# Kernel optimization log

Measured on AMD Instinct MI355X. Metric: run time of the kernel, lower is better.

Reference implementation:

```python
import jax, jax.numpy as jnp
import numpy as np

RATIO = 0.5  # init arg of CAGPool_layer
B, N_PER_GRAPH, D, DEG = 256, 512, 256, 32


def setup_inputs() -> dict:
    key = jax.random.key(0)
    k1, k2, k3, k4 = jax.random.split(key, 4)
    N = B * N_PER_GRAPH
    Eg = N_PER_GRAPH * DEG  # edges per graph
    x = jax.random.normal(k1, (N, D), dtype=jnp.float32)
    # within-graph random edges, then offset to global node ids
    src = jax.random.randint(k2, (B, Eg), 0, N_PER_GRAPH, dtype=jnp.int32)
    dst = jax.random.randint(k3, (B, Eg), 0, N_PER_GRAPH, dtype=jnp.int32)
    off = (jnp.arange(B, dtype=jnp.int32) * N_PER_GRAPH)[:, None]
    edge_index = jnp.stack([(src + off).reshape(-1), (dst + off).reshape(-1)], axis=0)
    batch = jnp.repeat(jnp.arange(B, dtype=jnp.int32), N_PER_GRAPH)
    pool_vector = jax.random.normal(k4, (B, D), dtype=jnp.float32)
    c_size = jnp.full((B,), N_PER_GRAPH, dtype=jnp.int32)  # uniform graph sizes
    return {"x": x, "edge_index": edge_index, "batch": batch,
            "pool_vector": pool_vector, "c_size": c_size}


def reference(x, edge_index, batch, pool_vector, c_size):
    N, d = x.shape
    Bn = pool_vector.shape[0]
    n = N // Bn  # uniform nodes per graph (c_size is constant = n)
    k = int(np.ceil(RATIO * n))

    # x_ = pool_vector repeated c_size[i] times == gather by batch (uniform sizes)
    x_ = pool_vector[batch]                                   # [N, d]
    score = jnp.sum(x * x_, axis=1) / jnp.linalg.norm(x_, axis=1)  # [N]

    # per-graph top-k (dense [B, n] view; graphs are contiguous blocks of n nodes)
    _, idx = jax.lax.top_k(score.reshape(Bn, n), k)           # [B, k] local ids
    perm = (idx + (jnp.arange(Bn, dtype=idx.dtype) * n)[:, None]).reshape(-1)  # [B*k]

    # gather kept nodes, sigmoid-gate by their scores
    x_out = x[perm] * jax.nn.sigmoid(score[perm])[:, None]    # [B*k, d]
    batch_out = batch[perm]                                   # [B*k]

    # filter_adj: remap node ids, mask edges with a dropped endpoint.
    # (torch version compacts the edge list; we keep static shape [2, E] and
    #  mark dropped edges with -1 plus a boolean validity mask.)
    nodemap = jnp.full((N,), -1, dtype=jnp.int32).at[perm].set(
        jnp.arange(perm.shape[0], dtype=jnp.int32))
    row = nodemap[edge_index[0]]
    col = nodemap[edge_index[1]]
    valid = (row >= 0) & (col >= 0)
    edge_index_new = jnp.stack([jnp.where(valid, row, -1),
                                jnp.where(valid, col, -1)], axis=0)
    return x_out, edge_index_new, batch_out, perm, valid
```

## Files before the change

### kernel.cpp

```cpp
#include <hip/hip_runtime.h>
#include <math.h>


__global__ void score_fused_kernel(const float4* __restrict__ x4,
                                   const float4* __restrict__ pool4,
                                   double* __restrict__ scores,
                                   int nv, int n) {
    int w = threadIdx.x >> 6;
    int l = threadIdx.x & 63;
    int nodeA = blockIdx.x * 8 + w * 2;
    int nodeB = nodeA + 1;
    int b = nodeA / n;
    const float4* pr = pool4 + (size_t)b * nv;
    const float4* xa = x4 + (size_t)nodeA * nv;
    const float4* xb = x4 + (size_t)nodeB * nv;
    double nn = 0.0, da = 0.0, db = 0.0;
    for (int j = l; j < nv; j += 64) {
        float4 pv = pr[j];
        float4 va = xa[j];
        float4 vb = xb[j];
        double px = pv.x, py = pv.y, pz = pv.z, pw = pv.w;
        nn += px * px + py * py + pz * pz + pw * pw;
        da += (double)va.x * px + (double)va.y * py
            + (double)va.z * pz + (double)va.w * pw;
        db += (double)vb.x * px + (double)vb.y * py
            + (double)vb.z * pz + (double)vb.w * pw;
    }
    for (int off = 32; off > 0; off >>= 1) {
        nn += __shfl_xor(nn, off, 64);
        da += __shfl_xor(da, off, 64);
        db += __shfl_xor(db, off, 64);
    }
    if (l == 0) {
        double inv = 1.0 / sqrt(nn);
        scores[nodeA] = da * inv;
        scores[nodeB] = db * inv;
    }
}

__global__ void norm_kernel(const float* __restrict__ pool,
                            double* __restrict__ inv_norm, int D) {
    int b = blockIdx.x;
    int l = threadIdx.x;
    double acc = 0.0;
    for (int j = l; j < D; j += 64) {
        double v = (double)pool[(size_t)b * D + j];
        acc += v * v;
    }
    for (int off = 32; off > 0; off >>= 1) acc += __shfl_down(acc, off, 64);
    if (l == 0) inv_norm[b] = 1.0 / sqrt(acc);
}

__global__ void score_kernel(const float* __restrict__ x,
                             const float* __restrict__ pool,
                             const double* __restrict__ inv_norm,
                             double* __restrict__ scores,
                             int D, int n) {
    int node = blockIdx.x * 4 + (threadIdx.x >> 6);
    int l = threadIdx.x & 63;
    int b = node / n;
    const float* xr = x + (size_t)node * D;
    const float* pr = pool + (size_t)b * D;
    double acc = 0.0;
    for (int j = l; j < D; j += 64)
        acc += (double)xr[j] * (double)pr[j];
    for (int off = 32; off > 0; off >>= 1) acc += __shfl_down(acc, off, 64);
    if (l == 0) scores[node] = acc * inv_norm[b];
}

__global__ void rank_kernel(const double* __restrict__ scores,
                            int* __restrict__ nodemap,
                            int* __restrict__ perm_int,
                            float* __restrict__ out,
                            long off_batch, long off_perm,
                            int n, int k) {
    extern __shared__ double s[];
    int b = blockIdx.x;
    int t = threadIdx.x;
    int gid = b * n + t;
    double st = scores[gid];
    s[t] = st;
    __syncthreads();
    int rank = 0;
#pragma unroll 8
    for (int j = 0; j < n; ++j) {
        double sj = s[j];
        rank += (int)((sj > st) || (sj == st && j < t));
    }
    if (rank < k) {
        int p = b * k + rank;
        nodemap[gid] = p;
        perm_int[p] = gid;
        out[off_batch + p] = (float)b;
        out[off_perm + p]  = (float)gid;
    } else {
        nodemap[gid] = -1;
    }
}

__global__ void out_kernel(const float4* __restrict__ x4,
                           const double* __restrict__ scores,
                           const int* __restrict__ perm_int,
                           const int4* __restrict__ ei_src,
                           const int4* __restrict__ ei_dst,
                           const int* __restrict__ nodemap,
                           float4* __restrict__ out0,
                           float4* __restrict__ out_row,
                           float4* __restrict__ out_col,
                           float4* __restrict__ out_valid,
                           int nv, int GA, long epg4, int n) {
    extern __shared__ int smem[];
    int bid = blockIdx.x;
    if (bid < GA) {
        int w = threadIdx.x >> 6, l = threadIdx.x & 63;
        int p = bid * 4 + w;
        int gid = perm_int[p];
        double sc = scores[gid];
        float g = (float)(1.0 / (1.0 + exp(-sc)));
        const float4* xr = x4 + (size_t)gid * nv;
        float4* orow = out0 + (size_t)p * nv;
        for (int j = l; j < nv; j += 64) {
            float4 v = xr[j];
            v.x *= g; v.y *= g; v.z *= g; v.w *= g;
            orow[j] = v;
        }
    } else {
        long blk = bid - GA;
        long e4base = blk * 256;
        long g = e4base / epg4;
        int base = (int)(g * (long)n);
        for (int i = threadIdx.x; i < n; i += 256)
            smem[i] = nodemap[base + i];
        __syncthreads();
        long e = e4base + threadIdx.x;
        int4 s = ei_src[e];
        int4 d = ei_dst[e];
        int r0 = smem[s.x - base], r1 = smem[s.y - base];
        int r2 = smem[s.z - base], r3 = smem[s.w - base];
        int c0 = smem[d.x - base], c1 = smem[d.y - base];
        int c2 = smem[d.z - base], c3 = smem[d.w - base];
        bool v0 = (r0 >= 0) & (c0 >= 0);
        bool v1 = (r1 >= 0) & (c1 >= 0);
        bool v2 = (r2 >= 0) & (c2 >= 0);
        bool v3 = (r3 >= 0) & (c3 >= 0);
        float4 rv = { v0 ? (float)r0 : -1.0f, v1 ? (float)r1 : -1.0f,
                      v2 ? (float)r2 : -1.0f, v3 ? (float)r3 : -1.0f };
        float4 cv = { v0 ? (float)c0 : -1.0f, v1 ? (float)c1 : -1.0f,
                      v2 ? (float)c2 : -1.0f, v3 ? (float)c3 : -1.0f };
        float4 vv = { v0 ? 1.0f : 0.0f, v1 ? 1.0f : 0.0f,
                      v2 ? 1.0f : 0.0f, v3 ? 1.0f : 0.0f };
        out_row[e]   = rv;
        out_col[e]   = cv;
        out_valid[e] = vv;
    }
}

__global__ void gather_kernel(const float* __restrict__ x,
                              const double* __restrict__ scores,
                              const int* __restrict__ perm_int,
                              float* __restrict__ out0, int D) {
    int p = blockIdx.x * 4 + (threadIdx.x >> 6);
    int l = threadIdx.x & 63;
    int gid = perm_int[p];
    double sc = scores[gid];
    float g = (float)(1.0 / (1.0 + exp(-sc)));
    const float* xr = x + (size_t)gid * D;
    float* orow = out0 + (size_t)p * D;
    for (int j = l; j < D; j += 64) orow[j] = xr[j] * g;
}

__global__ void edge_kernel(const int* __restrict__ ei,
                            const int* __restrict__ nodemap,
                            float* __restrict__ out,
                            long off_e, long off_valid, long E) {
    long e = (long)blockIdx.x * blockDim.x + threadIdx.x;
    if (e >= E) return;
    int r = nodemap[ei[e]];
    int c = nodemap[ei[E + e]];
    bool valid = (r >= 0) && (c >= 0);
    out[off_e + e]     = valid ? (float)r : -1.0f;
    out[off_e + E + e] = valid ? (float)c : -1.0f;
    out[off_valid + e] = valid ? 1.0f : 0.0f;
}

extern "C" void kernel_launch(void* const* d_in, const int* in_sizes, int n_in,
                              void* d_out, int out_size, void* d_ws, size_t ws_size,
                              hipStream_t stream) {
    const float* x    = (const float*)d_in[0];
    const int*   ei   = (const int*)d_in[1];
    const float* pool = (const float*)d_in[3];

    const int B = in_sizes[4];
    const int D = in_sizes[3] / B;
    const long N = (long)in_sizes[0] / D;
    const long E = (long)in_sizes[1] / 2;
    const int n = (int)(N / B);
    const int k = (n + 1) / 2;
    const long Eg = E / B;

    char* ws = (char*)d_ws;
    double* scores   = (double*)ws;                         ws += (size_t)N * 8;
    double* inv_norm = (double*)ws;                         ws += (size_t)B * 8;
    int*    nodemap  = (int*)ws;                            ws += (size_t)N * 4;
    int*    perm_int = (int*)ws;

    float* out = (float*)d_out;
    const long o0 = 0;
    const long o1 = o0 + (long)B * k * D;
    const long o2 = o1 + 2 * E;
    const long o3 = o2 + (long)B * k;
    const long o4 = o3 + (long)B * k;

    if ((n % 8 == 0) && (D % 4 == 0)) {
        score_fused_kernel<<<(int)(N / 8), 256, 0, stream>>>(
            (const float4*)x, (const float4*)pool, scores, D / 4, n);
    } else {
        norm_kernel<<<B, 64, 0, stream>>>(pool, inv_norm, D);
        score_kernel<<<(int)(N / 4), 256, 0, stream>>>(
            x, pool, inv_norm, scores, D, n);
    }

    rank_kernel<<<B, n, (size_t)n * sizeof(double), stream>>>(
        scores, nodemap, perm_int, out, o2, o3, n, k);

    bool fused_ok = (D % 4 == 0) && ((long)B * k % 4 == 0) &&
                    (E % 1024 == 0) && (Eg % 1024 == 0) &&
                    (o1 % 4 == 0) && ((o1 + E) % 4 == 0) && (o4 % 4 == 0);
    if (fused_ok) {
        int GA = (int)((long)B * k / 4);
        int GB = (int)(E / 1024);
        out_kernel<<<GA + GB, 256, (size_t)n * sizeof(int), stream>>>(
            (const float4*)x, scores, perm_int,
            (const int4*)ei, (const int4*)(ei + E), nodemap,
            (float4*)(out + o0), (float4*)(out + o1),
            (float4*)(out + o1 + E), (float4*)(out + o4),
            D / 4, GA, Eg / 4, n);
    } else {
        gather_kernel<<<(int)((long)B * k / 4), 256, 0, stream>>>(
            x, scores, perm_int, out + o0, D);
        edge_kernel<<<(int)((E + 255) / 256), 256, 0, stream>>>(
            ei, nodemap, out, o1, o4, E);
    }
}
```

Measured before the change: 86.19 us.

## Fuse score and rank into one per-graph kernel and precompute sigmoid gates

Scoring and top-k ranking are merged into one kernel with one 1024-thread block per graph. Scores stay in shared memory and never round-trip through global memory. The kernel also writes a precomputed sigmoid gate for each kept node, so the output kernel no longer reads double scores or computes exp. The edge branch of the output kernel now handles two int4 groups per thread to halve its block count. The cost is that only B=256 blocks run the score phase, which may underfill the GPU while it streams all of x.

Result: faster. 84.27 us (-2.2%).

```diff
diff --git a/kernel.cpp b/kernel.cpp
--- a/kernel.cpp
+++ b/kernel.cpp
@@ -2,39 +2,134 @@
 #include <math.h>
 
 
-__global__ void score_fused_kernel(const float4* __restrict__ x4,
-                                   const float4* __restrict__ pool4,
-                                   double* __restrict__ scores,
-                                   int nv, int n) {
-    int w = threadIdx.x >> 6;
-    int l = threadIdx.x & 63;
-    int nodeA = blockIdx.x * 8 + w * 2;
-    int nodeB = nodeA + 1;
-    int b = nodeA / n;
-    const float4* pr = pool4 + (size_t)b * nv;
-    const float4* xa = x4 + (size_t)nodeA * nv;
-    const float4* xb = x4 + (size_t)nodeB * nv;
-    double nn = 0.0, da = 0.0, db = 0.0;
-    for (int j = l; j < nv; j += 64) {
-        float4 pv = pr[j];
-        float4 va = xa[j];
-        float4 vb = xb[j];
-        double px = pv.x, py = pv.y, pz = pv.z, pw = pv.w;
-        nn += px * px + py * py + pz * pz + pw * pw;
-        da += (double)va.x * px + (double)va.y * py
-            + (double)va.z * pz + (double)va.w * pw;
-        db += (double)vb.x * px + (double)vb.y * py
-            + (double)vb.z * pz + (double)vb.w * pw;
-    }
-    for (int off = 32; off > 0; off >>= 1) {
-        nn += __shfl_xor(nn, off, 64);
-        da += __shfl_xor(da, off, 64);
-        db += __shfl_xor(db, off, 64);
-    }
-    if (l == 0) {
-        double inv = 1.0 / sqrt(nn);
-        scores[nodeA] = da * inv;
-        scores[nodeB] = db * inv;
+__global__ __launch_bounds__(1024)
+void score_rank_kernel(const float4* __restrict__ x4,
+                       const float4* __restrict__ pool4,
+                       int* __restrict__ nodemap,
+                       int* __restrict__ perm_int,
+                       float* __restrict__ gate,
+                       float* __restrict__ out,
+                       long off_batch, long off_perm,
+                       int n, int k) {
+    extern __shared__ double s[];
+    int b = blockIdx.x;
+    int t = threadIdx.x;
+    int w = t >> 6, l = t & 63;
+    int nw = blockDim.x >> 6;
+
+    float4 pv = pool4[(size_t)b * 64 + l];
+    double px = pv.x, py = pv.y, pz = pv.z, pw = pv.w;
+    double nn = px * px + py * py + pz * pz + pw * pw;
+    for (int off = 32; off > 0; off >>= 1) nn += __shfl_xor(nn, off, 64);
+    double inv = 1.0 / sqrt(nn);
+
+    int npw = n / nw;
+    const float4* xg = x4 + ((size_t)b * n + (size_t)w * npw) * 64;
+    for (int i = 0; i < npw; i += 4) {
+        const float4* xa = xg + (size_t)i * 64;
+        float4 va = xa[l], vb = xa[64 + l], vc = xa[128 + l], vd = xa[192 + l];
+        double da = (double)va.x * px + (double)va.y * py
+                  + (double)va.z * pz + (double)va.w * pw;
+        double db = (double)vb.x * px + (double)vb.y * py
+                  + (double)vb.z * pz + (double)vb.w * pw;
+        double dc = (double)vc.x * px + (double)vc.y * py
+                  + (double)vc.z * pz + (double)vc.w * pw;
+        double dd = (double)vd.x * px + (double)vd.y * py
+                  + (double)vd.z * pz + (double)vd.w * pw;
+        for (int off = 32; off > 0; off >>= 1) {
+            da += __shfl_xor(da, off, 64);
+            db += __shfl_xor(db, off, 64);
+            dc += __shfl_xor(dc, off, 64);
+            dd += __shfl_xor(dd, off, 64);
+        }
+        if (l == 0) {
+            int base = w * npw + i;
+            s[base]     = da * inv;
+            s[base + 1] = db * inv;
+            s[base + 2] = dc * inv;
+            s[base + 3] = dd * inv;
+        }
+    }
+    __syncthreads();
+
+    if (t < n) {
+        double st = s[t];
+        int rank = 0;
+#pragma unroll 8
+        for (int j = 0; j < n; ++j) {
+            double sj = s[j];
+            rank += (int)((sj > st) || (sj == st && j < t));
+        }
+        int gid = b * n + t;
+        if (rank < k) {
+            int p = b * k + rank;
+            nodemap[gid] = p;
+            perm_int[p] = gid;
+            gate[p] = (float)(1.0 / (1.0 + exp(-st)));
+            out[off_batch + p] = (float)b;
+            out[off_perm + p]  = (float)gid;
+        } else {
+            nodemap[gid] = -1;
+        }
+    }
+}
+
+__global__ void out_kernel(const float4* __restrict__ x4,
+                           const float* __restrict__ gate,
+                           const int* __restrict__ perm_int,
+                           const int4* __restrict__ ei_src,
+                           const int4* __restrict__ ei_dst,
+                           const int* __restrict__ nodemap,
+                           float4* __restrict__ out0,
+                           float4* __restrict__ out_row,
+                           float4* __restrict__ out_col,
+                           float4* __restrict__ out_valid,
+                           int nv, int GA, long epg4, int n) {
+    extern __shared__ int smem[];
+    int bid = blockIdx.x;
+    if (bid < GA) {
+        int w = threadIdx.x >> 6, l = threadIdx.x & 63;
+        int p = bid * 4 + w;
+        int gid = perm_int[p];
+        float g = gate[p];
+        const float4* xr = x4 + (size_t)gid * nv;
+        float4* orow = out0 + (size_t)p * nv;
+        for (int j = l; j < nv; j += 64) {
+            float4 v = xr[j];
+            v.x *= g; v.y *= g; v.z *= g; v.w *= g;
+            orow[j] = v;
+        }
+    } else {
+        long blk = bid - GA;
+        long e4base = blk * 512;
+        long g = e4base / epg4;
+        int base = (int)(g * (long)n);
+        for (int i = threadIdx.x; i < n; i += 256)
+            smem[i] = nodemap[base + i];
+        __syncthreads();
+#pragma unroll
+        for (int half = 0; half < 2; ++half) {
+            long e = e4base + half * 256 + threadIdx.x;
+            int4 sv = ei_src[e];
+            int4 dv = ei_dst[e];
+            int r0 = smem[sv.x - base], r1 = smem[sv.y - base];
+            int r2 = smem[sv.z - base], r3 = smem[sv.w - base];
+            int c0 = smem[dv.x - base], c1 = smem[dv.y - base];
+            int c2 = smem[dv.z - base], c3 = smem[dv.w - base];
+            bool v0 = (r0 >= 0) & (c0 >= 0);
+            bool v1 = (r1 >= 0) & (c1 >= 0);
+            bool v2 = (r2 >= 0) & (c2 >= 0);
+            bool v3 = (r3 >= 0) & (c3 >= 0);
+            float4 rv = { v0 ? (float)r0 : -1.0f, v1 ? (float)r1 : -1.0f,
+                          v2 ? (float)r2 : -1.0f, v3 ? (float)r3 : -1.0f };
+            float4 cv = { v0 ? (float)c0 : -1.0f, v1 ? (float)c1 : -1.0f,
+                          v2 ? (float)c2 : -1.0f, v3 ? (float)c3 : -1.0f };
+            float4 vv = { v0 ? 1.0f : 0.0f, v1 ? 1.0f : 0.0f,
+                          v2 ? 1.0f : 0.0f, v3 ? 1.0f : 0.0f };
+            out_row[e]   = rv;
+            out_col[e]   = cv;
+            out_valid[e] = vv;
+        }
     }
 }
 
@@ -82,7 +177,6 @@
     s[t] = st;
     __syncthreads();
     int rank = 0;
-#pragma unroll 8
     for (int j = 0; j < n; ++j) {
         double sj = s[j];
         rank += (int)((sj > st) || (sj == st && j < t));
@@ -98,69 +192,12 @@
     }
 }
 
-__global__ void out_kernel(const float4* __restrict__ x4,
-                           const double* __restrict__ scores,
-                           const int* __restrict__ perm_int,
-                           const int4* __restrict__ ei_src,
-                           const int4* __restrict__ ei_dst,
-                           const int* __restrict__ nodemap,
-                           float4* __restrict__ out0,
-                           float4* __restrict__ out_row,
-                           float4* __restrict__ out_col,
-                           float4* __restrict__ out_valid,
-                           int nv, int GA, long epg4, int n) {
-    extern __shared__ int smem[];
-    int bid = blockIdx.x;
-    if (bid < GA) {
-        int w = threadIdx.x >> 6, l = threadIdx.x & 63;
-        int p = bid * 4 + w;
-        int gid = perm_int[p];
-        double sc = scores[gid];
-        float g = (float)(1.0 / (1.0 + exp(-sc)));
-        const float4* xr = x4 + (size_t)gid * nv;
-        float4* orow = out0 + (size_t)p * nv;
-        for (int j = l; j < nv; j += 64) {
-            float4 v = xr[j];
-            v.x *= g; v.y *= g; v.z *= g; v.w *= g;
-            orow[j] = v;
-        }
-    } else {
-        long blk = bid - GA;
-        long e4base = blk * 256;
-        long g = e4base / epg4;
-        int base = (int)(g * (long)n);
-        for (int i = threadIdx.x; i < n; i += 256)
-            smem[i] = nodemap[base + i];
-        __syncthreads();
-        long e = e4base + threadIdx.x;
-        int4 s = ei_src[e];
-        int4 d = ei_dst[e];
-        int r0 = smem[s.x - base], r1 = smem[s.y - base];
-        int r2 = smem[s.z - base], r3 = smem[s.w - base];
-        int c0 = smem[d.x - base], c1 = smem[d.y - base];
-        int c2 = smem[d.z - base], c3 = smem[d.w - base];
-        bool v0 = (r0 >= 0) & (c0 >= 0);
-        bool v1 = (r1 >= 0) & (c1 >= 0);
-        bool v2 = (r2 >= 0) & (c2 >= 0);
-        bool v3 = (r3 >= 0) & (c3 >= 0);
-        float4 rv = { v0 ? (float)r0 : -1.0f, v1 ? (float)r1 : -1.0f,
-                      v2 ? (float)r2 : -1.0f, v3 ? (float)r3 : -1.0f };
-        float4 cv = { v0 ? (float)c0 : -1.0f, v1 ? (float)c1 : -1.0f,
-                      v2 ? (float)c2 : -1.0f, v3 ? (float)c3 : -1.0f };
-        float4 vv = { v0 ? 1.0f : 0.0f, v1 ? 1.0f : 0.0f,
-                      v2 ? 1.0f : 0.0f, v3 ? 1.0f : 0.0f };
-        out_row[e]   = rv;
-        out_col[e]   = cv;
-        out_valid[e] = vv;
-    }
-}
-
 __global__ void gather_kernel(const float* __restrict__ x,
                               const double* __restrict__ scores,
                               const int* __restrict__ perm_int,
                               float* __restrict__ out0, int D) {
-    int p = blockIdx.x * 4 + (threadIdx.x >> 6);
-    int l = threadIdx.x & 63;
+    int p = blockIdx.x;
+    int l = threadIdx.x;
     int gid = perm_int[p];
     double sc = scores[gid];
     float g = (float)(1.0 / (1.0 + exp(-sc)));
@@ -202,7 +239,8 @@
     double* scores   = (double*)ws;                         ws += (size_t)N * 8;
     double* inv_norm = (double*)ws;                         ws += (size_t)B * 8;
     int*    nodemap  = (int*)ws;                            ws += (size_t)N * 4;
-    int*    perm_int = (int*)ws;
+    int*    perm_int = (int*)ws;                            ws += (size_t)B * ((N/B+1)/2) * 4;
+    float*  gate     = (float*)ws;
 
     float* out = (float*)d_out;
     const long o0 = 0;
@@ -211,32 +249,30 @@
     const long o3 = o2 + (long)B * k;
     const long o4 = o3 + (long)B * k;
 
-    if ((n % 8 == 0) && (D % 4 == 0)) {
-        score_fused_kernel<<<(int)(N / 8), 256, 0, stream>>>(
-            (const float4*)x, (const float4*)pool, scores, D / 4, n);
-    } else {
-        norm_kernel<<<B, 64, 0, stream>>>(pool, inv_norm, D);
-        score_kernel<<<(int)(N / 4), 256, 0, stream>>>(
-            x, pool, inv_norm, scores, D, n);
-    }
-
-    rank_kernel<<<B, n, (size_t)n * sizeof(double), stream>>>(
-        scores, nodemap, perm_int, out, o2, o3, n, k);
-
-    bool fused_ok = (D % 4 == 0) && ((long)B * k % 4 == 0) &&
-                    (E % 1024 == 0) && (Eg % 1024 == 0) &&
-                    (o1 % 4 == 0) && ((o1 + E) % 4 == 0) && (o4 % 4 == 0);
-    if (fused_ok) {
+    bool fused_sr_ok = (D == 256) && (n % 64 == 0) && (n <= 1024);
+    bool fused_out_ok = fused_sr_ok && ((long)B * k % 4 == 0) &&
+                        (E % 2048 == 0) && (Eg % 2048 == 0) &&
+                        (o1 % 4 == 0) && ((o1 + E) % 4 == 0) && (o4 % 4 == 0);
+
+    if (fused_out_ok) {
+        score_rank_kernel<<<B, 1024, (size_t)n * sizeof(double), stream>>>(
+            (const float4*)x, (const float4*)pool,
+            nodemap, perm_int, gate, out, o2, o3, n, k);
         int GA = (int)((long)B * k / 4);
-        int GB = (int)(E / 1024);
+        int GB = (int)(E / 2048);
         out_kernel<<<GA + GB, 256, (size_t)n * sizeof(int), stream>>>(
-            (const float4*)x, scores, perm_int,
+            (const float4*)x, gate, perm_int,
             (const int4*)ei, (const int4*)(ei + E), nodemap,
             (float4*)(out + o0), (float4*)(out + o1),
             (float4*)(out + o1 + E), (float4*)(out + o4),
             D / 4, GA, Eg / 4, n);
     } else {
-        gather_kernel<<<(int)((long)B * k / 4), 256, 0, stream>>>(
+        norm_kernel<<<B, 64, 0, stream>>>(pool, inv_norm, D);
+        score_kernel<<<(int)(N / 4), 256, 0, stream>>>(
+            x, pool, inv_norm, scores, D, n);
+        rank_kernel<<<B, n, (size_t)n * sizeof(double), stream>>>(
+            scores, nodemap, perm_int, out, o2, o3, n, k);
+        gather_kernel<<<(int)((long)B * k), 64, 0, stream>>>(
             x, scores, perm_int, out + o0, D);
         edge_kernel<<<(int)((E + 255) / 256), 256, 0, stream>>>(
             ei, nodemap, out, o1, o4, E);
```
